# Kernel tuning notes

Measured on AMD Instinct MI355X. Metric: run time of the kernel, lower is better.

## Reference

```python
import jax, jax.numpy as jnp
import numpy as np

# NEURONSv2 config defaults (assumed from NEURONSv2Config)
DT = 1.0            # simulation step (ms)
TAU_MEM = 20.0      # membrane time constant
TAU_SYN = 5.0       # synaptic time constant
TAU_DEND = 10.0     # dendritic time constant
THRESHOLD = 1.0     # spike threshold, reset_mechanism='subtract'
DEND_COUPLING = 0.5 # dendritic coupling strength
NAT_FREQ = 10.0     # oscillator natural frequency (Hz)
OSC_K = 1.0         # Kuramoto coupling strength
OSC_DT = 0.001      # oscillator integration step (s)
SPIKE_GAIN = 1.0    # spike drive into phase dynamics
TWO_PI = 2.0 * np.pi


def spike_fn(v):
    """Heaviside spike with sigmoid surrogate gradient (straight-through)."""
    s_hard = (v > 0).astype(v.dtype)
    s_soft = jax.nn.sigmoid(4.0 * v)
    return s_soft + jax.lax.stop_gradient(s_hard - s_soft)


def setup_inputs() -> dict:
    B, T, I, O = 32, 4096, 256, 256
    NB, NA = 4, 2  # n_basal, n_apical dendrites
    key = jax.random.key(0)
    k1, k2, k3, k4 = jax.random.split(key, 4)
    scale = 1.0 / np.sqrt(I)
    return {
        "x": jax.random.normal(k1, (B, T, I), dtype=jnp.float32),
        "W_soma": jax.random.normal(k2, (O, I), dtype=jnp.float32) * scale,
        "W_basal": jax.random.normal(k3, (NB, O, I), dtype=jnp.float32) * scale,
        "W_apical": jax.random.normal(k4, (NA, O, I), dtype=jnp.float32) * scale,
    }


def reference(x, W_soma, W_basal, W_apical):
    B, T, I = x.shape
    O = W_soma.shape[0]
    dt = jnp.float32(DT)
    a_mem = jnp.exp(-dt / TAU_MEM)
    a_syn = jnp.exp(-dt / TAU_SYN)
    a_dend = jnp.exp(-dt / TAU_DEND)

    def step(carry, x_t):
        mem, syn, dend, theta = carry
        # dendritic computation: nonlinear branch integration, low-pass filtered
        basal = jax.nn.relu(jnp.einsum('bi,noi->bno', x_t, W_basal)).mean(axis=1)   # [B,O]
        apical = jax.nn.relu(jnp.einsum('bi,noi->bno', x_t, W_apical)).mean(axis=1)  # [B,O]
        dend = a_dend * dend + (1.0 - a_dend) * (basal + apical)
        soma = x_t @ W_soma.T                                                        # [B,O]
        drive = soma + DEND_COUPLING * dend
        # LIF dynamics
        syn = a_syn * syn + drive
        mem = a_mem * mem + syn
        spikes = spike_fn(mem - THRESHOLD)
        mem = mem - spikes * THRESHOLD  # reset by subtraction
        # Kuramoto mean-field phase update
        c = jnp.cos(theta).mean(axis=-1, keepdims=True)
        s = jnp.sin(theta).mean(axis=-1, keepdims=True)
        r = jnp.sqrt(c * c + s * s)
        psi = jnp.arctan2(s, c)
        dtheta = TWO_PI * NAT_FREQ + OSC_K * r * jnp.sin(psi - theta) + SPIKE_GAIN * spikes
        theta = jnp.mod(theta + OSC_DT * dtheta, TWO_PI)
        return (mem, syn, dend, theta), (spikes, theta, mem)

    zeros = jnp.zeros((B, O), dtype=x.dtype)
    init = (zeros, zeros, zeros, zeros)
    _, (spk, ph, mm) = jax.lax.scan(step, init, jnp.swapaxes(x, 0, 1))
    # [T,B,O] -> [B,T,O]
    spikes = jnp.swapaxes(spk, 0, 1)
    phases = jnp.swapaxes(ph, 0, 1)
    membrane = jnp.swapaxes(mm, 0, 1)
    return spikes, phases, membrane
```

## Files before the change

### kernel.cpp

```cpp
#include <hip/hip_runtime.h>
#include <cstdint>
#include <cstddef>

#define BD 32
#define TD 4096
#define ID 256
#define OD 256

#define A_DEND 0.90483741803595957f
#define A_SYN  0.81873075307798182f
#define A_MEM  0.95122942450071402f
#define TWO_PI_F 6.28318530717958647692f
#define BASE_DTH 62.8318530717958647692f
#define INV256 0.00390625f

#define DOT4(acc, xv, wv)               \
  acc = fmaf((xv).x, (wv).x, acc);      \
  acc = fmaf((xv).y, (wv).y, acc);      \
  acc = fmaf((xv).z, (wv).z, acc);      \
  acc = fmaf((xv).w, (wv).w, acc);


#define WSTR 260
#define XROWSTR 68
#define XCHF (64 * XROWSTR)

__global__ __launch_bounds__(512, 1)
void proj_kernel(const float* __restrict__ x,
                 const float* __restrict__ Ws,
                 const float* __restrict__ Wb,
                 const float* __restrict__ Wa,
                 float* __restrict__ soma_ws,
                 float* __restrict__ u_ws) {
  #pragma clang fp contract(off)
  __shared__ float wl[112 * WSTR];
  __shared__ float xcf[2 * XCHF];

  const int tid = threadIdx.x;
  const int lin = (int)blockIdx.x + ((int)blockIdx.y << 4);
  const int swz = ((lin & 7) << 7) + (lin >> 3);
  const int o0  = (swz & 15) << 4;
  const int by  = swz >> 4;

  for (int rep = 0; rep < 14; ++rep) {
    int f = (rep << 9) + tid;
    int r = f >> 6;
    int c = (f & 63) << 2;
    const float* src;
    if (r < 16) {
      src = Ws + (((size_t)(o0 + r)) << 8);
    } else if (r < 80) {
      src = Wb + (((size_t)((((r - 16) >> 4) << 8) + o0 + (r & 15))) << 8);
    } else {
      src = Wa + (((size_t)((((r - 80) >> 4) << 8) + o0 + (r & 15))) << 8);
    }
    *(float4*)(&wl[r * WSTR + c]) = *(const float4*)(src + c);
  }

  const int oo = tid & 15;
  const int mr = (tid >> 4) << 1;
  const float* w0p = wl + (  0 + oo) * WSTR;
  const float* w1p = wl + ( 16 + oo) * WSTR;
  const float* w2p = wl + ( 32 + oo) * WSTR;
  const float* w3p = wl + ( 48 + oo) * WSTR;
  const float* w4p = wl + ( 64 + oo) * WSTR;
  const float* w5p = wl + ( 80 + oo) * WSTR;
  const float* w6p = wl + ( 96 + oo) * WSTR;

  const int f0 = tid, f1 = tid + 512;
  const int sr0 = f0 >> 4, sc0 = (f0 & 15) << 2;
  const int sr1 = f1 >> 4, sc1 = (f1 & 15) << 2;
  const int d0 = sr0 * XROWSTR + sc0;
  const int d1 = sr1 * XROWSTR + sc1;

  const size_t trow0 = ((size_t)by) << 11;

  {
    *(float4*)(&xcf[d0]) = *(const float4*)(x + (trow0 + sr0) * ID + sc0);
    *(float4*)(&xcf[d1]) = *(const float4*)(x + (trow0 + sr1) * ID + sc1);
  }
  __syncthreads();

  for (int mt = 0; mt < 32; ++mt) {
    const size_t row0 = trow0 + ((size_t)mt << 6);
    float acS[2]  = {0.f, 0.f}, acB0[2] = {0.f, 0.f}, acB1[2] = {0.f, 0.f},
          acB2[2] = {0.f, 0.f}, acB3[2] = {0.f, 0.f}, acA0[2] = {0.f, 0.f},
          acA1[2] = {0.f, 0.f};
    #pragma unroll
    for (int kc = 0; kc < 4; ++kc) {
      float4 pa = {0.f, 0.f, 0.f, 0.f}, pb = {0.f, 0.f, 0.f, 0.f};
      const bool hn = !(kc == 3 && mt == 31);
      if (hn) {
        const size_t nrow = (kc < 3) ? row0 : (row0 + 64);
        const int nk = (kc < 3) ? ((kc + 1) << 6) : 0;
        pa = *(const float4*)(x + (nrow + sr0) * ID + nk + sc0);
        pb = *(const float4*)(x + (nrow + sr1) * ID + nk + sc1);
      }
      const float* xA = xcf + ((kc & 1) ? XCHF : 0) + mr * XROWSTR;
      const float* xB = xA + XROWSTR;
      #pragma unroll 4
      for (int kk = 0; kk < 64; kk += 4) {
        float4 xv0 = *(const float4*)(xA + kk);
        float4 xv1 = *(const float4*)(xB + kk);
        float4 vs  = *(const float4*)(w0p + (kc << 6) + kk);
        float4 vb0 = *(const float4*)(w1p + (kc << 6) + kk);
        float4 vb1 = *(const float4*)(w2p + (kc << 6) + kk);
        float4 vb2 = *(const float4*)(w3p + (kc << 6) + kk);
        float4 vb3 = *(const float4*)(w4p + (kc << 6) + kk);
        float4 va0 = *(const float4*)(w5p + (kc << 6) + kk);
        float4 va1 = *(const float4*)(w6p + (kc << 6) + kk);
        DOT4(acS[0], xv0, vs)   DOT4(acS[1], xv1, vs)
        DOT4(acB0[0], xv0, vb0) DOT4(acB0[1], xv1, vb0)
        DOT4(acB1[0], xv0, vb1) DOT4(acB1[1], xv1, vb1)
        DOT4(acB2[0], xv0, vb2) DOT4(acB2[1], xv1, vb2)
        DOT4(acB3[0], xv0, vb3) DOT4(acB3[1], xv1, vb3)
        DOT4(acA0[0], xv0, va0) DOT4(acA0[1], xv1, va0)
        DOT4(acA1[0], xv0, va1) DOT4(acA1[1], xv1, va1)
      }
      if (hn) {
        float* dst = xcf + (((kc & 1) ^ 1) ? XCHF : 0);
        *(float4*)(dst + d0) = pa;
        *(float4*)(dst + d1) = pb;
      }
      __syncthreads();
    }
    const size_t mb = (row0 + mr) * OD + (o0 + oo);
    #pragma unroll
    for (int j = 0; j < 2; ++j) {
      float bm = ((fmaxf(acB0[j], 0.f) + fmaxf(acB1[j], 0.f)) +
                  (fmaxf(acB2[j], 0.f) + fmaxf(acB3[j], 0.f))) * 0.25f;
      float am = (fmaxf(acA0[j], 0.f) + fmaxf(acA1[j], 0.f)) * 0.5f;
      soma_ws[mb + (size_t)j * OD] = acS[j];
      u_ws[mb + (size_t)j * OD]    = bm + am;
    }
  }
}


#define DPP_ADD(v, ctrl, rm, bm, bc)                                          \
  v += __builtin_bit_cast(float, __builtin_amdgcn_update_dpp(                 \
           0, __builtin_bit_cast(int, v), ctrl, rm, bm, bc));

__device__ __forceinline__ float wave_sum64(float v) {
  DPP_ADD(v, 0x111, 0xf, 0xf, true)
  DPP_ADD(v, 0x112, 0xf, 0xf, true)
  DPP_ADD(v, 0x114, 0xf, 0xf, true)
  DPP_ADD(v, 0x118, 0xf, 0xf, true)
  DPP_ADD(v, 0x142, 0xa, 0xf, false)
  DPP_ADD(v, 0x143, 0xc, 0xf, false)
  return __builtin_bit_cast(float, __builtin_amdgcn_readlane(__builtin_bit_cast(int, v), 63));
}

#define PROCESS4(TBASE)                                                       \
  _Pragma("unroll")                                                           \
  for (int i = 0; i < 4; ++i) {                                               \
    const int t = (TBASE) + i;                                                \
    const float* sv = &cs[i].x;                                               \
    const float* uv = &cu[i].x;                                               \
    float spk[4], cc[4], ss[4];                                               \
    _Pragma("unroll")                                                         \
    for (int j = 0; j < 4; ++j) {                                             \
      float t1 = A_DEND * dend[j];                                            \
      float t2 = bD * uv[j];                                                  \
      dend[j] = t1 + t2;                                                      \
      float drive = sv[j] + 0.5f * dend[j];                                   \
      syn[j] = (A_SYN * syn[j]) + drive;                                      \
      mem[j] = (A_MEM * mem[j]) + syn[j];                                     \
      float v = mem[j] - 1.0f;                                                \
      float sp = (v > 0.0f) ? 1.0f : 0.0f;                                    \
      mem[j] = mem[j] - sp;                                                   \
      spk[j] = sp;                                                            \
      cc[j] = __cosf(th[j]);                                                  \
      ss[j] = __sinf(th[j]);                                                  \
    }                                                                         \
    float csum = (cc[0] + cc[1]) + (cc[2] + cc[3]);                           \
    float ssum = (ss[0] + ss[1]) + (ss[2] + ss[3]);                           \
    float cS = wave_sum64(csum);                                              \
    float sS = wave_sum64(ssum);                                              \
    _Pragma("unroll")                                                         \
    for (int j = 0; j < 4; ++j) {                                             \
      float coup = (sS * cc[j] - cS * ss[j]) * INV256;                        \
      float dth = (BASE_DTH + coup) + spk[j];                                 \
      th[j] = th[j] + 0.001f * dth;                                           \
      th[j] = (th[j] >= TWO_PI_F) ? (th[j] - TWO_PI_F) : th[j];               \
    }                                                                         \
    float4 so = {spk[0], spk[1], spk[2], spk[3]};                             \
    float4 po = {th[0], th[1], th[2], th[3]};                                 \
    float4 mo = {mem[0], mem[1], mem[2], mem[3]};                             \
    Os[(size_t)t * 64] = so;                                                  \
    Op[(size_t)t * 64] = po;                                                  \
    Om[(size_t)t * 64] = mo;                                                  \
  }

__global__ __launch_bounds__(64, 1)
void dyn_kernel(const float* __restrict__ soma_ws,
                const float* __restrict__ u_ws,
                float* __restrict__ out) {
  #pragma clang fp contract(off)
  const int b = blockIdx.x;
  const int l = threadIdx.x;

  const size_t base4 = ((size_t)b << 18) + l;
  const float4* S = (const float4*)soma_ws + base4;
  const float4* U = (const float4*)u_ws + base4;
  float4* Os = (float4*)out + base4;
  float4* Op = Os + ((size_t)1 << 23);
  float4* Om = Op + ((size_t)1 << 23);

  float dend[4] = {0.f, 0.f, 0.f, 0.f};
  float syn[4]  = {0.f, 0.f, 0.f, 0.f};
  float mem[4]  = {0.f, 0.f, 0.f, 0.f};
  float th[4]   = {0.f, 0.f, 0.f, 0.f};

  const float bD = 1.0f - A_DEND;

  float4 As[4], Au[4], Bs[4], Bu[4];
  #pragma unroll
  for (int i = 0; i < 4; ++i) { As[i] = S[(size_t)i * 64];       Au[i] = U[(size_t)i * 64]; }
  #pragma unroll
  for (int i = 0; i < 4; ++i) { Bs[i] = S[(size_t)(4 + i) * 64]; Bu[i] = U[(size_t)(4 + i) * 64]; }

  for (int t8 = 0; t8 < TD / 8; ++t8) {
    float4 cs[4], cu[4];
    #pragma unroll
    for (int i = 0; i < 4; ++i) { cs[i] = As[i]; cu[i] = Au[i]; }
    if (t8 < TD / 8 - 1) {
      #pragma unroll
      for (int i = 0; i < 4; ++i) {
        As[i] = S[(size_t)((t8 << 3) + 8 + i) * 64];
        Au[i] = U[(size_t)((t8 << 3) + 8 + i) * 64];
      }
    }
    PROCESS4((t8 << 3));
    #pragma unroll
    for (int i = 0; i < 4; ++i) { cs[i] = Bs[i]; cu[i] = Bu[i]; }
    if (t8 < TD / 8 - 1) {
      #pragma unroll
      for (int i = 0; i < 4; ++i) {
        Bs[i] = S[(size_t)((t8 << 3) + 12 + i) * 64];
        Bu[i] = U[(size_t)((t8 << 3) + 12 + i) * 64];
      }
    }
    PROCESS4((t8 << 3) + 4);
  }
}


extern "C" void kernel_launch(void* const* d_in, const int* in_sizes, int n_in,
                              void* d_out, int out_size, void* d_ws, size_t ws_size,
                              hipStream_t stream) {
  const float* x  = (const float*)d_in[0];
  const float* Ws = (const float*)d_in[1];
  const float* Wb = (const float*)d_in[2];
  const float* Wa = (const float*)d_in[3];

  float* soma_ws = (float*)d_ws;
  float* u_ws    = soma_ws + (size_t)BD * TD * OD;
  float* out     = (float*)d_out;

  dim3 gA(16, 64, 1);
  proj_kernel<<<gA, 512, 0, stream>>>(x, Ws, Wb, Wa, soma_ws, u_ws);
  dyn_kernel<<<BD, 64, 0, stream>>>(soma_ws, u_ws, out);
}
```

Before: 3.694 ms.

## Enlarge register tile in projection GEMM and pack dynamics waves into fewer blocks

The projection kernel moves from a 2-row by 1-output register tile per thread to an 8-row by 2-output tile over 7 weight matrices, with 112 accumulators per thread. It processes the 2048-row segment in four 512-row passes, using 8-wide k chunks that are double-buffered in shared memory. The goal is more FMA work per LDS load and fewer shared-memory reads for each FLOP, at the cost of heavy register pressure and possible spills. Separately, the dynamics kernel now runs as 4 blocks of 512 threads instead of 32 single-wave blocks, which puts 8 waves on each CU and may change memory-latency hiding for the serial scan.

```diff
diff --git a/kernel.cpp b/kernel.cpp
--- a/kernel.cpp
+++ b/kernel.cpp
@@ -22,8 +22,8 @@
 
 
 #define WSTR 260
-#define XROWSTR 68
-#define XCHF (64 * XROWSTR)
+#define XMGSTR 68
+#define XBUFF (64 * XMGSTR)
 
 __global__ __launch_bounds__(512, 1)
 void proj_kernel(const float* __restrict__ x,
@@ -34,7 +34,7 @@
                  float* __restrict__ u_ws) {
   #pragma clang fp contract(off)
   __shared__ float wl[112 * WSTR];
-  __shared__ float xcf[2 * XCHF];
+  __shared__ float xs[2 * XBUFF];
 
   const int tid = threadIdx.x;
   const int lin = (int)blockIdx.x + ((int)blockIdx.y << 4);
@@ -57,81 +57,87 @@
     *(float4*)(&wl[r * WSTR + c]) = *(const float4*)(src + c);
   }
 
-  const int oo = tid & 15;
-  const int mr = (tid >> 4) << 1;
-  const float* w0p = wl + (  0 + oo) * WSTR;
-  const float* w1p = wl + ( 16 + oo) * WSTR;
-  const float* w2p = wl + ( 32 + oo) * WSTR;
-  const float* w3p = wl + ( 48 + oo) * WSTR;
-  const float* w4p = wl + ( 64 + oo) * WSTR;
-  const float* w5p = wl + ( 80 + oo) * WSTR;
-  const float* w6p = wl + ( 96 + oo) * WSTR;
-
-  const int f0 = tid, f1 = tid + 512;
-  const int sr0 = f0 >> 4, sc0 = (f0 & 15) << 2;
-  const int sr1 = f1 >> 4, sc1 = (f1 & 15) << 2;
-  const int d0 = sr0 * XROWSTR + sc0;
-  const int d1 = sr1 * XROWSTR + sc1;
+  const int oo = tid & 7;
+  const int mg = tid >> 3;
+  const float* wpp[7];
+  #pragma unroll
+  for (int p = 0; p < 7; ++p) wpp[p] = wl + (((p << 4) + (oo << 1)) * WSTR);
+
+  const int row0 = tid >> 1;
+  const int cc   = (tid & 1) << 2;
+  const int d0   = (row0 >> 3) * XMGSTR + (row0 & 7) * 8 + cc;
+  const int d1   = ((row0 >> 3) + 32) * XMGSTR + (row0 & 7) * 8 + cc;
 
   const size_t trow0 = ((size_t)by) << 11;
 
   {
-    *(float4*)(&xcf[d0]) = *(const float4*)(x + (trow0 + sr0) * ID + sc0);
-    *(float4*)(&xcf[d1]) = *(const float4*)(x + (trow0 + sr1) * ID + sc1);
+    float4 a = *(const float4*)(x + (trow0 + row0) * ID + cc);
+    float4 b = *(const float4*)(x + (trow0 + row0 + 256) * ID + cc);
+    *(float4*)(&xs[d0]) = a;
+    *(float4*)(&xs[d1]) = b;
   }
   __syncthreads();
 
-  for (int mt = 0; mt < 32; ++mt) {
-    const size_t row0 = trow0 + ((size_t)mt << 6);
-    float acS[2]  = {0.f, 0.f}, acB0[2] = {0.f, 0.f}, acB1[2] = {0.f, 0.f},
-          acB2[2] = {0.f, 0.f}, acB3[2] = {0.f, 0.f}, acA0[2] = {0.f, 0.f},
-          acA1[2] = {0.f, 0.f};
-    #pragma unroll
-    for (int kc = 0; kc < 4; ++kc) {
+  for (int pass = 0; pass < 4; ++pass) {
+    float acc[7][16];
+    #pragma unroll
+    for (int p = 0; p < 7; ++p) {
+      #pragma unroll
+      for (int j = 0; j < 16; ++j) acc[p][j] = 0.f;
+    }
+
+    for (int ck = 0; ck < 32; ++ck) {
+      const int k0 = ck << 3;
       float4 pa = {0.f, 0.f, 0.f, 0.f}, pb = {0.f, 0.f, 0.f, 0.f};
-      const bool hn = !(kc == 3 && mt == 31);
+      const bool hn = !(pass == 3 && ck == 31);
       if (hn) {
-        const size_t nrow = (kc < 3) ? row0 : (row0 + 64);
-        const int nk = (kc < 3) ? ((kc + 1) << 6) : 0;
-        pa = *(const float4*)(x + (nrow + sr0) * ID + nk + sc0);
-        pb = *(const float4*)(x + (nrow + sr1) * ID + nk + sc1);
-      }
-      const float* xA = xcf + ((kc & 1) ? XCHF : 0) + mr * XROWSTR;
-      const float* xB = xA + XROWSTR;
-      #pragma unroll 4
-      for (int kk = 0; kk < 64; kk += 4) {
-        float4 xv0 = *(const float4*)(xA + kk);
-        float4 xv1 = *(const float4*)(xB + kk);
-        float4 vs  = *(const float4*)(w0p + (kc << 6) + kk);
-        float4 vb0 = *(const float4*)(w1p + (kc << 6) + kk);
-        float4 vb1 = *(const float4*)(w2p + (kc << 6) + kk);
-        float4 vb2 = *(const float4*)(w3p + (kc << 6) + kk);
-        float4 vb3 = *(const float4*)(w4p + (kc << 6) + kk);
-        float4 va0 = *(const float4*)(w5p + (kc << 6) + kk);
-        float4 va1 = *(const float4*)(w6p + (kc << 6) + kk);
-        DOT4(acS[0], xv0, vs)   DOT4(acS[1], xv1, vs)
-        DOT4(acB0[0], xv0, vb0) DOT4(acB0[1], xv1, vb0)
-        DOT4(acB1[0], xv0, vb1) DOT4(acB1[1], xv1, vb1)
-        DOT4(acB2[0], xv0, vb2) DOT4(acB2[1], xv1, vb2)
-        DOT4(acB3[0], xv0, vb3) DOT4(acB3[1], xv1, vb3)
-        DOT4(acA0[0], xv0, va0) DOT4(acA0[1], xv1, va0)
-        DOT4(acA1[0], xv0, va1) DOT4(acA1[1], xv1, va1)
+        const int cn = (pass << 5) + ck + 1;
+        const size_t rb = trow0 + ((size_t)(cn >> 5) << 9);
+        const int kn = (cn & 31) << 3;
+        pa = *(const float4*)(x + (rb + row0) * ID + kn + cc);
+        pb = *(const float4*)(x + (rb + row0 + 256) * ID + kn + cc);
+      }
+      const float* xb = xs + ((ck & 1) ? XBUFF : 0) + mg * XMGSTR;
+      #pragma unroll
+      for (int q = 0; q < 2; ++q) {
+        float4 xv[8];
+        #pragma unroll
+        for (int r = 0; r < 8; ++r) xv[r] = *(const float4*)(xb + r * 8 + (q << 2));
+        const int ko = k0 + (q << 2);
+        #pragma unroll
+        for (int p = 0; p < 7; ++p) {
+          float4 w0 = *(const float4*)(wpp[p] + ko);
+          float4 w1 = *(const float4*)(wpp[p] + WSTR + ko);
+          #pragma unroll
+          for (int r = 0; r < 8; ++r) {
+            DOT4(acc[p][r], xv[r], w0)
+            DOT4(acc[p][8 + r], xv[r], w1)
+          }
+        }
       }
       if (hn) {
-        float* dst = xcf + (((kc & 1) ^ 1) ? XCHF : 0);
-        *(float4*)(dst + d0) = pa;
-        *(float4*)(dst + d1) = pb;
+        float* d = xs + ((ck & 1) ? 0 : XBUFF);
+        *(float4*)(d + d0) = pa;
+        *(float4*)(d + d1) = pb;
       }
       __syncthreads();
     }
-    const size_t mb = (row0 + mr) * OD + (o0 + oo);
-    #pragma unroll
-    for (int j = 0; j < 2; ++j) {
-      float bm = ((fmaxf(acB0[j], 0.f) + fmaxf(acB1[j], 0.f)) +
-                  (fmaxf(acB2[j], 0.f) + fmaxf(acB3[j], 0.f))) * 0.25f;
-      float am = (fmaxf(acA0[j], 0.f) + fmaxf(acA1[j], 0.f)) * 0.5f;
-      soma_ws[mb + (size_t)j * OD] = acS[j];
-      u_ws[mb + (size_t)j * OD]    = bm + am;
+
+    const size_t rbase = trow0 + ((size_t)pass << 9) + ((size_t)mg << 3);
+    const int ocol = o0 + (oo << 1);
+    #pragma unroll
+    for (int r = 0; r < 8; ++r) {
+      const size_t off = (rbase + r) * OD + ocol;
+      float bm0 = ((fmaxf(acc[1][r], 0.f) + fmaxf(acc[2][r], 0.f)) +
+                   (fmaxf(acc[3][r], 0.f) + fmaxf(acc[4][r], 0.f))) * 0.25f;
+      float am0 = (fmaxf(acc[5][r], 0.f) + fmaxf(acc[6][r], 0.f)) * 0.5f;
+      float bm1 = ((fmaxf(acc[1][8 + r], 0.f) + fmaxf(acc[2][8 + r], 0.f)) +
+                   (fmaxf(acc[3][8 + r], 0.f) + fmaxf(acc[4][8 + r], 0.f))) * 0.25f;
+      float am1 = (fmaxf(acc[5][8 + r], 0.f) + fmaxf(acc[6][8 + r], 0.f)) * 0.5f;
+      float2 sv = {acc[0][r], acc[0][8 + r]};
+      float2 uv = {bm0 + am0, bm1 + am1};
+      *(float2*)(soma_ws + off) = sv;
+      *(float2*)(u_ws + off)    = uv;
     }
   }
 }
@@ -192,13 +198,13 @@
     Om[(size_t)t * 64] = mo;                                                  \
   }
 
-__global__ __launch_bounds__(64, 1)
+__global__ __launch_bounds__(512, 1)
 void dyn_kernel(const float* __restrict__ soma_ws,
                 const float* __restrict__ u_ws,
                 float* __restrict__ out) {
   #pragma clang fp contract(off)
-  const int b = blockIdx.x;
-  const int l = threadIdx.x;
+  const int b = (int)blockIdx.x * 8 + ((int)threadIdx.x >> 6);
+  const int l = threadIdx.x & 63;
 
   const size_t base4 = ((size_t)b << 18) + l;
   const float4* S = (const float4*)soma_ws + base4;
@@ -260,5 +266,5 @@
 
   dim3 gA(16, 64, 1);
   proj_kernel<<<gA, 512, 0, stream>>>(x, Ws, Wb, Wa, soma_ws, u_ws);
-  dyn_kernel<<<BD, 64, 0, stream>>>(soma_ws, u_ws, out);
-}
+  dyn_kernel<<<4, 512, 0, stream>>>(soma_ws, u_ws, out);
+}
```

Measured after the change: 8.747 ms. 2.37x slower.

## Restructure projection GEMM with 8x7 register tiles and direct global-to-LDS loads

Applied to the files above, without the earlier changes.

The projection kernel now gives each thread 8 rows by 7 weight projections, up from 2 rows, so each weight value read from shared memory is reused across more rows. Loading of x and the weights now uses global_load_lds to copy straight into shared memory, skipping register staging. The grid changes from 1024 blocks, each walking 2048 rows, to 8192 blocks that each handle one 256-row slab, with a new block-to-tile mapping. The costs are more accumulator registers (56 per thread), 8x more weight reloads into shared memory in total, and a different synchronisation pattern with double buffering.

```diff
diff --git a/kernel.cpp b/kernel.cpp
--- a/kernel.cpp
+++ b/kernel.cpp
@@ -20,10 +20,15 @@
   acc = fmaf((xv).z, (wv).z, acc);      \
   acc = fmaf((xv).w, (wv).w, acc);
 
+__device__ __forceinline__ void gload_lds16(const float* g, float* l) {
+  __builtin_amdgcn_global_load_lds(
+      (const __attribute__((address_space(1))) unsigned int*)g,
+      (__attribute__((address_space(3))) unsigned int*)l,
+      16, 0, 0);
+}
+
 
 #define WSTR 260
-#define XROWSTR 68
-#define XCHF (64 * XROWSTR)
 
 __global__ __launch_bounds__(512, 1)
 void proj_kernel(const float* __restrict__ x,
@@ -34,18 +39,22 @@
                  float* __restrict__ u_ws) {
   #pragma clang fp contract(off)
   __shared__ float wl[112 * WSTR];
-  __shared__ float xcf[2 * XCHF];
+  __shared__ float xsf[2 * 4096];
 
   const int tid = threadIdx.x;
-  const int lin = (int)blockIdx.x + ((int)blockIdx.y << 4);
-  const int swz = ((lin & 7) << 7) + (lin >> 3);
-  const int o0  = (swz & 15) << 4;
-  const int by  = swz >> 4;
-
+  const int l   = tid & 63;
+  const int w   = tid >> 6;
+
+  const int bid    = (int)blockIdx.x;
+  const int slot   = bid >> 3;
+  const int family = ((slot >> 4) << 3) + (bid & 7);
+  const int within = slot & 15;
+  const int o0     = within << 4;
+  const int slab0  = family << 8;
+
+  #pragma unroll
   for (int rep = 0; rep < 14; ++rep) {
-    int f = (rep << 9) + tid;
-    int r = f >> 6;
-    int c = (f & 63) << 2;
+    const int r = (rep << 3) + w;
     const float* src;
     if (r < 16) {
       src = Ws + (((size_t)(o0 + r)) << 8);
@@ -54,85 +63,71 @@
     } else {
       src = Wa + (((size_t)((((r - 80) >> 4) << 8) + o0 + (r & 15))) << 8);
     }
-    *(float4*)(&wl[r * WSTR + c]) = *(const float4*)(src + c);
-  }
+    gload_lds16(src + (l << 2), wl + r * WSTR);
+  }
+
+  const float4* g0 = (const float4*)x + ((size_t)(slab0 + (tid >> 2)) << 6) + (tid & 3);
+  const float4* g1 = g0 + (128 << 6);
+  const int wb4 = ((tid >> 6) << 6) << 2;
+  gload_lds16((const float*)g0, xsf + wb4);
+  gload_lds16((const float*)g1, xsf + wb4 + 2048);
 
   const int oo = tid & 15;
-  const int mr = (tid >> 4) << 1;
-  const float* w0p = wl + (  0 + oo) * WSTR;
-  const float* w1p = wl + ( 16 + oo) * WSTR;
-  const float* w2p = wl + ( 32 + oo) * WSTR;
-  const float* w3p = wl + ( 48 + oo) * WSTR;
-  const float* w4p = wl + ( 64 + oo) * WSTR;
-  const float* w5p = wl + ( 80 + oo) * WSTR;
-  const float* w6p = wl + ( 96 + oo) * WSTR;
-
-  const int f0 = tid, f1 = tid + 512;
-  const int sr0 = f0 >> 4, sc0 = (f0 & 15) << 2;
-  const int sr1 = f1 >> 4, sc1 = (f1 & 15) << 2;
-  const int d0 = sr0 * XROWSTR + sc0;
-  const int d1 = sr1 * XROWSTR + sc1;
-
-  const size_t trow0 = ((size_t)by) << 11;
-
-  {
-    *(float4*)(&xcf[d0]) = *(const float4*)(x + (trow0 + sr0) * ID + sc0);
-    *(float4*)(&xcf[d1]) = *(const float4*)(x + (trow0 + sr1) * ID + sc1);
-  }
+  const int mg = tid >> 4;
+  const float* wA = wl + oo * WSTR;
+  const float* wB = wA + 4 * 16 * WSTR;
+  const float* xbf = xsf + (mg << 4);
+
+  float acc[7][8];
+  #pragma unroll
+  for (int p = 0; p < 7; ++p) {
+    #pragma unroll
+    for (int r = 0; r < 8; ++r) acc[p][r] = 0.f;
+  }
+
   __syncthreads();
 
-  for (int mt = 0; mt < 32; ++mt) {
-    const size_t row0 = trow0 + ((size_t)mt << 6);
-    float acS[2]  = {0.f, 0.f}, acB0[2] = {0.f, 0.f}, acB1[2] = {0.f, 0.f},
-          acB2[2] = {0.f, 0.f}, acB3[2] = {0.f, 0.f}, acA0[2] = {0.f, 0.f},
-          acA1[2] = {0.f, 0.f};
-    #pragma unroll
-    for (int kc = 0; kc < 4; ++kc) {
-      float4 pa = {0.f, 0.f, 0.f, 0.f}, pb = {0.f, 0.f, 0.f, 0.f};
-      const bool hn = !(kc == 3 && mt == 31);
-      if (hn) {
-        const size_t nrow = (kc < 3) ? row0 : (row0 + 64);
-        const int nk = (kc < 3) ? ((kc + 1) << 6) : 0;
-        pa = *(const float4*)(x + (nrow + sr0) * ID + nk + sc0);
-        pb = *(const float4*)(x + (nrow + sr1) * ID + nk + sc1);
-      }
-      const float* xA = xcf + ((kc & 1) ? XCHF : 0) + mr * XROWSTR;
-      const float* xB = xA + XROWSTR;
-      #pragma unroll 4
-      for (int kk = 0; kk < 64; kk += 4) {
-        float4 xv0 = *(const float4*)(xA + kk);
-        float4 xv1 = *(const float4*)(xB + kk);
-        float4 vs  = *(const float4*)(w0p + (kc << 6) + kk);
-        float4 vb0 = *(const float4*)(w1p + (kc << 6) + kk);
-        float4 vb1 = *(const float4*)(w2p + (kc << 6) + kk);
-        float4 vb2 = *(const float4*)(w3p + (kc << 6) + kk);
-        float4 vb3 = *(const float4*)(w4p + (kc << 6) + kk);
-        float4 va0 = *(const float4*)(w5p + (kc << 6) + kk);
-        float4 va1 = *(const float4*)(w6p + (kc << 6) + kk);
-        DOT4(acS[0], xv0, vs)   DOT4(acS[1], xv1, vs)
-        DOT4(acB0[0], xv0, vb0) DOT4(acB0[1], xv1, vb0)
-        DOT4(acB1[0], xv0, vb1) DOT4(acB1[1], xv1, vb1)
-        DOT4(acB2[0], xv0, vb2) DOT4(acB2[1], xv1, vb2)
-        DOT4(acB3[0], xv0, vb3) DOT4(acB3[1], xv1, vb3)
-        DOT4(acA0[0], xv0, va0) DOT4(acA0[1], xv1, va0)
-        DOT4(acA1[0], xv0, va1) DOT4(acA1[1], xv1, va1)
-      }
-      if (hn) {
-        float* dst = xcf + (((kc & 1) ^ 1) ? XCHF : 0);
-        *(float4*)(dst + d0) = pa;
-        *(float4*)(dst + d1) = pb;
-      }
-      __syncthreads();
-    }
-    const size_t mb = (row0 + mr) * OD + (o0 + oo);
-    #pragma unroll
-    for (int j = 0; j < 2; ++j) {
-      float bm = ((fmaxf(acB0[j], 0.f) + fmaxf(acB1[j], 0.f)) +
-                  (fmaxf(acB2[j], 0.f) + fmaxf(acB3[j], 0.f))) * 0.25f;
-      float am = (fmaxf(acA0[j], 0.f) + fmaxf(acA1[j], 0.f)) * 0.5f;
-      soma_ws[mb + (size_t)j * OD] = acS[j];
-      u_ws[mb + (size_t)j * OD]    = bm + am;
-    }
+#define K4GROUP(XOFF, WOFF)                                                \
+  _Pragma("unroll")                                                        \
+  for (int q = 0; q < 4; ++q) {                                            \
+    float4 xv[8];                                                          \
+    _Pragma("unroll")                                                      \
+    for (int r = 0; r < 8; ++r)                                            \
+      xv[r] = *(const float4*)(xbf + (XOFF) + r * 512 + (q << 2));         \
+    _Pragma("unroll")                                                      \
+    for (int p = 0; p < 7; ++p) {                                          \
+      const float* wp = (p < 4) ? (wA + p * 16 * WSTR)                     \
+                                : (wB + (p - 4) * 16 * WSTR);              \
+      float4 wv = *(const float4*)(wp + (WOFF) + (q << 2));                \
+      DOT4(acc[p][0], xv[0], wv) DOT4(acc[p][1], xv[1], wv)                \
+      DOT4(acc[p][2], xv[2], wv) DOT4(acc[p][3], xv[3], wv)                \
+      DOT4(acc[p][4], xv[4], wv) DOT4(acc[p][5], xv[5], wv)                \
+      DOT4(acc[p][6], xv[6], wv) DOT4(acc[p][7], xv[7], wv)                \
+    }                                                                      \
+  }
+
+  for (int c = 0; c < 8; ++c) {
+    gload_lds16((const float*)(g0 + 4), xsf + 4096 + wb4);
+    gload_lds16((const float*)(g1 + 4), xsf + 4096 + wb4 + 2048);
+    K4GROUP(0, 0)
+    __syncthreads();
+    if (c < 7) {
+      gload_lds16((const float*)(g0 + 8), xsf + wb4);
+      gload_lds16((const float*)(g1 + 8), xsf + wb4 + 2048);
+    }
+    K4GROUP(4096, 16)
+    __syncthreads();
+    wA += 32; wB += 32; g0 += 8; g1 += 8;
+  }
+
+  #pragma unroll
+  for (int r = 0; r < 8; ++r) {
+    const size_t off = (((size_t)slab0 + mg + (r << 5)) << 8) + o0 + oo;
+    float bm = ((fmaxf(acc[1][r], 0.f) + fmaxf(acc[2][r], 0.f)) +
+                (fmaxf(acc[3][r], 0.f) + fmaxf(acc[4][r], 0.f))) * 0.25f;
+    float am = (fmaxf(acc[5][r], 0.f) + fmaxf(acc[6][r], 0.f)) * 0.5f;
+    soma_ws[off] = acc[0][r];
+    u_ws[off]    = bm + am;
   }
 }
 
@@ -258,7 +253,6 @@
   float* u_ws    = soma_ws + (size_t)BD * TD * OD;
   float* out     = (float*)d_out;
 
-  dim3 gA(16, 64, 1);
-  proj_kernel<<<gA, 512, 0, stream>>>(x, Ws, Wb, Wa, soma_ws, u_ws);
+  proj_kernel<<<8192, 512, 0, stream>>>(x, Ws, Wb, Wa, soma_ws, u_ws);
   dyn_kernel<<<BD, 64, 0, stream>>>(soma_ws, u_ws, out);
 }
```

New measurement: 4.815 ms. +30.4%, slower.
